# Performance work log

Measured on AMD Instinct MI355X. Metric: run time of the kernel, lower is better.

The kernel has to match this reference:

```python
import jax, jax.numpy as jnp
import numpy as np

B, CQ, CKV, H, W = 16, 512, 512, 48, 48
NH = 8
HD = CQ // NH
SCALE = HD ** -0.5


def setup_inputs() -> dict:
    key = jax.random.key(0)
    ks = jax.random.split(key, 11)
    s = 0.02
    return {
        "query_features": jax.random.normal(ks[0], (B, CQ, H, W), jnp.float32),
        "key_features": jax.random.normal(ks[1], (B, CKV, H, W), jnp.float32),
        "value_features": jax.random.normal(ks[2], (B, CKV, H, W), jnp.float32),
        "Wq": jax.random.normal(ks[3], (CQ, CQ), jnp.float32) * s,
        "bq": jnp.zeros((CQ,), jnp.float32),
        "Wk": jax.random.normal(ks[4], (CQ, CKV), jnp.float32) * s,
        "bk": jnp.zeros((CQ,), jnp.float32),
        "Wv": jax.random.normal(ks[5], (CQ, CKV), jnp.float32) * s,
        "bv": jnp.zeros((CQ,), jnp.float32),
        "Wo": jax.random.normal(ks[6], (CQ, CQ), jnp.float32) * s,
        "bo": jnp.zeros((CQ,), jnp.float32),
    }


def _proj(x, Wt, b):
    # 1x1 conv == channel GEMM: (O,C) x (B,C,H,W) -> (B,O,H,W)
    return jnp.einsum('oc,bchw->bohw', Wt, x) + b[None, :, None, None]


def reference(query_features, key_features, value_features,
              Wq, bq, Wk, bk, Wv, bv, Wo, bo):
    b, cq, h, w = query_features.shape
    hw = h * w
    Q = _proj(query_features, Wq, bq).reshape(b, NH, HD, hw)
    K = _proj(key_features, Wk, bk).reshape(b, NH, HD, hw)
    V = _proj(value_features, Wv, bv).reshape(b, NH, HD, hw)
    # NOTE: faithful to source — contraction is over the SPATIAL axis d=H*W,
    # so scores are (B, NH, HD, HD) (head_dim x head_dim attention).
    scores = jnp.einsum('bnhd,bnkd->bnhk', Q, K) * SCALE
    attn = jax.nn.softmax(scores, axis=-1)
    out = jnp.einsum('bnhk,bnkd->bnhd', attn, V)  # (B, NH, HD, HW)
    out = out.reshape(b, cq, h, w)
    return _proj(out, Wo, bo)
```

## Files before the change

### kernel.cpp

```cpp
#include <hip/hip_runtime.h>
#include <hip/hip_bf16.h>

#define B_   16
#define C_   512
#define HW_  2304
#define NH_  8
#define HD_  64
#define SCALE_ 0.125f

typedef __bf16 bf16x8 __attribute__((ext_vector_type(8)));
typedef __bf16 bf16x4 __attribute__((ext_vector_type(4)));
typedef float  f32x4  __attribute__((ext_vector_type(4)));

#define MFMA16(a, b, c) __builtin_amdgcn_mfma_f32_16x16x32_bf16((a), (b), (c), 0, 0, 0)

__device__ __forceinline__ void gload_lds16(const void* g, void* l) {
    __builtin_amdgcn_global_load_lds(
        (const __attribute__((address_space(1))) unsigned int*)g,
        (__attribute__((address_space(3))) unsigned int*)l, 16, 0, 0);
}

__global__ __launch_bounds__(256) void prep(
    const float* __restrict__ X, __bf16* __restrict__ XT,
    const float* __restrict__ W, __bf16* __restrict__ Wb)
{
    const int t = threadIdx.x;
    if (blockIdx.z == 16) {
        const int bid = blockIdx.y * 18 + blockIdx.x;
        if (bid < 128) {
            const int idx = bid * 2048 + t * 8;
            const float4 f0 = *(const float4*)&W[idx];
            const float4 f1 = *(const float4*)&W[idx + 4];
            bf16x8 o;
            o[0] = (__bf16)f0.x; o[1] = (__bf16)f0.y; o[2] = (__bf16)f0.z; o[3] = (__bf16)f0.w;
            o[4] = (__bf16)f1.x; o[5] = (__bf16)f1.y; o[6] = (__bf16)f1.z; o[7] = (__bf16)f1.w;
            *(bf16x8*)&Wb[idx] = o;
        }
        return;
    }
    const int b  = blockIdx.z;
    const int c0 = blockIdx.y * 64;
    const int h0 = blockIdx.x * 128;
    const float* Xb = X + (size_t)b * C_ * HW_;
    __bf16* XTb = XT + (size_t)b * HW_ * C_;

    __shared__ float Ts[64 * 129];

    #pragma unroll
    for (int p = 0; p < 8; ++p) {
        const int c  = p * 8 + (t >> 5);
        const int hg = (t & 31) * 4;
        const float4 v = *(const float4*)&Xb[(size_t)(c0 + c) * HW_ + h0 + hg];
        Ts[c * 129 + hg + 0] = v.x;
        Ts[c * 129 + hg + 1] = v.y;
        Ts[c * 129 + hg + 2] = v.z;
        Ts[c * 129 + hg + 3] = v.w;
    }
    __syncthreads();
    #pragma unroll
    for (int p = 0; p < 4; ++p) {
        const int hw = p * 32 + (t >> 3);
        const int g  = (t & 7) * 8;
        bf16x8 o;
        #pragma unroll
        for (int e = 0; e < 8; ++e)
            o[e] = (__bf16)Ts[(g + e) * 129 + hw];
        *(bf16x8*)&XTb[(size_t)(h0 + hw) * C_ + c0 + g] = o;
    }
}

template <typename OUT_T>
__device__ __forceinline__ void gemm_body(
    const __bf16* __restrict__ XTb, const __bf16* __restrict__ Wb,
    const float* __restrict__ bias, OUT_T* __restrict__ Yb,
    int n0, int m0)
{
    __shared__ __align__(16) __bf16 As[128 * 64];
    __shared__ __align__(16) __bf16 Bs[128 * 64];

    const int t = threadIdx.x;
    const int w = t >> 6, lane = t & 63, l16 = lane & 15, q = lane >> 4;
    const int wm = w >> 1, wn = w & 1;
    const int sr = lane >> 3;
    const int sg = ((lane & 7) ^ (lane >> 3)) * 8;

    f32x4 acc[4][4] = {};

    for (int ks = 0; ks < 8; ++ks) {
        const int k0 = ks * 64;
        __syncthreads();
        #pragma unroll
        for (int p = 0; p < 4; ++p) {
            const int rb = p * 32 + w * 8;
            gload_lds16(&Wb [(size_t)(m0 + rb + sr) * C_ + k0 + sg], &As[rb * 64]);
            gload_lds16(&XTb[(size_t)(n0 + rb + sr) * C_ + k0 + sg], &Bs[rb * 64]);
        }
        __syncthreads();
        #pragma unroll
        for (int kk = 0; kk < 2; ++kk) {
            const int sw = ((kk * 4 + q) ^ (l16 & 7)) * 8;
            bf16x8 af[4], bfr[4];
            #pragma unroll
            for (int mi = 0; mi < 4; ++mi)
                af[mi] = *(bf16x8*)&As[(wm * 64 + mi * 16 + l16) * 64 + sw];
            #pragma unroll
            for (int ni = 0; ni < 4; ++ni)
                bfr[ni] = *(bf16x8*)&Bs[(wn * 64 + ni * 16 + l16) * 64 + sw];
            #pragma unroll
            for (int mi = 0; mi < 4; ++mi)
                #pragma unroll
                for (int ni = 0; ni < 4; ++ni)
                    acc[mi][ni] = MFMA16(af[mi], bfr[ni], acc[mi][ni]);
        }
    }

    #pragma unroll
    for (int mi = 0; mi < 4; ++mi) {
        #pragma unroll
        for (int r = 0; r < 4; ++r) {
            const int m = m0 + wm * 64 + mi * 16 + q * 4 + r;
            const float bv_ = bias[m];
            #pragma unroll
            for (int ni = 0; ni < 4; ++ni) {
                const int n = n0 + wn * 64 + ni * 16 + l16;
                Yb[(size_t)m * HW_ + n] = (OUT_T)(acc[mi][ni][r] + bv_);
            }
        }
    }
}

__global__ __launch_bounds__(256) void proj_gemm(
    const __bf16* __restrict__ XT, const __bf16* __restrict__ Wb,
    const float* __restrict__ bias, __bf16* __restrict__ Y)
{
    const int b = blockIdx.z;
    gemm_body<__bf16>(XT + (size_t)b * HW_ * C_, Wb, bias,
                      Y + (size_t)b * C_ * HW_, blockIdx.x * 128, blockIdx.y * 128);
}

__global__ __launch_bounds__(256) void proj_out(
    const __bf16* __restrict__ AOT, const __bf16* __restrict__ Wb,
    const float* __restrict__ bias, float* __restrict__ out)
{
    const int b = blockIdx.z;
    gemm_body<float>(AOT + (size_t)b * HW_ * C_, Wb, bias,
                     out + (size_t)b * C_ * HW_, blockIdx.x * 128, blockIdx.y * 128);
}

__global__ __launch_bounds__(256) void attn_scores_part(
    const __bf16* __restrict__ Qw, const __bf16* __restrict__ Kw,
    float* __restrict__ Sp)
{
    const int bn  = blockIdx.x;
    const int kcs = blockIdx.y;
    const __bf16* Qb = Qw + (size_t)bn * 64 * HW_;
    const __bf16* Kb = Kw + (size_t)bn * 64 * HW_;

    __shared__ __align__(16) __bf16 Qs[64 * 64];
    __shared__ __align__(16) __bf16 Ks[64 * 64];

    const int t    = threadIdx.x;
    const int w    = t >> 6;
    const int lane = t & 63;
    const int l16  = lane & 15;
    const int q    = lane >> 4;
    const int sr   = lane >> 3;
    const int sg   = ((lane & 7) ^ (lane >> 3)) * 8;

    f32x4 acc[4] = {};

    for (int it = 0; it < 9; ++it) {
        const int k0 = kcs * 576 + it * 64;
        __syncthreads();
        #pragma unroll
        for (int p = 0; p < 2; ++p) {
            const int rb = w * 16 + p * 8;
            gload_lds16(&Qb[(size_t)(rb + sr) * HW_ + k0 + sg], &Qs[rb * 64]);
            gload_lds16(&Kb[(size_t)(rb + sr) * HW_ + k0 + sg], &Ks[rb * 64]);
        }
        __syncthreads();
        #pragma unroll
        for (int kk = 0; kk < 2; ++kk) {
            const int sw = ((kk * 4 + q) ^ (l16 & 7)) * 8;
            const bf16x8 a = *(bf16x8*)&Qs[(w * 16 + l16) * 64 + sw];
            #pragma unroll
            for (int ni = 0; ni < 4; ++ni) {
                const bf16x8 bb = *(bf16x8*)&Ks[(ni * 16 + l16) * 64 + sw];
                acc[ni] = MFMA16(a, bb, acc[ni]);
            }
        }
    }

    float* S = Sp + ((size_t)kcs * 128 + bn) * 4096;
    #pragma unroll
    for (int r = 0; r < 4; ++r)
        #pragma unroll
        for (int ni = 0; ni < 4; ++ni)
            S[(w * 16 + q * 4 + r) * 64 + ni * 16 + l16] = acc[ni][r];
}

__global__ __launch_bounds__(256) void softmax_reduce(
    const float* __restrict__ Sp, __bf16* __restrict__ Pw)
{
    const int bn = blockIdx.x;
    const int t  = threadIdx.x;
    const int r  = t >> 2;
    const int c0 = (t & 3) * 16;

    float v[16];
    #pragma unroll
    for (int j = 0; j < 16; ++j) v[j] = 0.f;
    #pragma unroll
    for (int kc = 0; kc < 4; ++kc) {
        const float* s = Sp + ((size_t)kc * 128 + bn) * 4096 + r * 64 + c0;
        #pragma unroll
        for (int j4 = 0; j4 < 4; ++j4) {
            const float4 f = *(const float4*)&s[j4 * 4];
            v[j4 * 4 + 0] += f.x; v[j4 * 4 + 1] += f.y;
            v[j4 * 4 + 2] += f.z; v[j4 * 4 + 3] += f.w;
        }
    }
    float mx = -1e30f;
    #pragma unroll
    for (int j = 0; j < 16; ++j) { v[j] *= SCALE_; mx = fmaxf(mx, v[j]); }
    mx = fmaxf(mx, __shfl_xor(mx, 1));
    mx = fmaxf(mx, __shfl_xor(mx, 2));
    float s = 0.f;
    #pragma unroll
    for (int j = 0; j < 16; ++j) { v[j] = __expf(v[j] - mx); s += v[j]; }
    s += __shfl_xor(s, 1);
    s += __shfl_xor(s, 2);
    const float inv = 1.f / s;
    bf16x8 o0, o1;
    #pragma unroll
    for (int j = 0; j < 8; ++j) {
        o0[j] = (__bf16)(v[j] * inv);
        o1[j] = (__bf16)(v[8 + j] * inv);
    }
    *(bf16x8*)&Pw[(size_t)bn * 4096 + r * 64 + c0]     = o0;
    *(bf16x8*)&Pw[(size_t)bn * 4096 + r * 64 + c0 + 8] = o1;
}

__global__ __launch_bounds__(256) void attn_pv(
    const __bf16* __restrict__ Pw, const __bf16* __restrict__ Vw,
    __bf16* __restrict__ AOT, const float* __restrict__ Wo, __bf16* __restrict__ WoB)
{
    const int t = threadIdx.x;
    if (blockIdx.x == 9) {
        const int idx = blockIdx.y * 2048 + t * 8;
        const float4 f0 = *(const float4*)&Wo[idx];
        const float4 f1 = *(const float4*)&Wo[idx + 4];
        bf16x8 o;
        o[0] = (__bf16)f0.x; o[1] = (__bf16)f0.y; o[2] = (__bf16)f0.z; o[3] = (__bf16)f0.w;
        o[4] = (__bf16)f1.x; o[5] = (__bf16)f1.y; o[6] = (__bf16)f1.z; o[7] = (__bf16)f1.w;
        *(bf16x8*)&WoB[idx] = o;
        return;
    }
    const int dsl = blockIdx.x;
    const int bn  = blockIdx.y;
    const int w    = t >> 6;
    const int lane = t & 63;
    const int l16  = lane & 15;
    const int q    = lane >> 4;

    __shared__ __align__(16) __bf16 Ps[64 * 72];
    __shared__ __align__(16) __bf16 Vt[4][16 * 264];

    {
        const int row = t >> 2;
        const int kc  = (t & 3) * 16;
        *(bf16x8*)&Ps[row * 72 + kc]     = *(const bf16x8*)&Pw[(size_t)bn * 4096 + row * 64 + kc];
        *(bf16x8*)&Ps[row * 72 + kc + 8] = *(const bf16x8*)&Pw[(size_t)bn * 4096 + row * 64 + kc + 8];
    }

    const __bf16* Vb = Vw + (size_t)bn * 64 * HW_;
    const int d0w = dsl * 256 + w * 64;
    {
        const int m4 = lane & 15;
        const int kh = (lane >> 4) * 16;
        __bf16 rr[4][16];
        #pragma unroll
        for (int j = 0; j < 16; ++j) {
            const bf16x4 v = *(const bf16x4*)&Vb[(size_t)(kh + j) * HW_ + d0w + 4 * m4];
            #pragma unroll
            for (int e = 0; e < 4; ++e) rr[e][j] = v[e];
        }
        #pragma unroll
        for (int e = 0; e < 4; ++e) {
            bf16x8 s0, s1;
            #pragma unroll
            for (int j = 0; j < 8; ++j) { s0[j] = rr[e][j]; s1[j] = rr[e][8 + j]; }
            *(bf16x8*)&Vt[w][m4 * 264 + e * 64 + kh]     = s0;
            *(bf16x8*)&Vt[w][m4 * 264 + e * 64 + kh + 8] = s1;
        }
    }
    __syncthreads();

    f32x4 acc[4][4] = {};
    #pragma unroll
    for (int kk = 0; kk < 2; ++kk) {
        bf16x8 af[4], bfr[4];
        #pragma unroll
        for (int mi = 0; mi < 4; ++mi)
            af[mi] = *(bf16x8*)&Ps[(mi * 16 + l16) * 72 + kk * 32 + q * 8];
        #pragma unroll
        for (int ni = 0; ni < 4; ++ni) {
            const int dl = ni * 16 + l16;
            bfr[ni] = *(bf16x8*)&Vt[w][(dl >> 2) * 264 + (dl & 3) * 64 + kk * 32 + q * 8];
        }
        #pragma unroll
        for (int mi = 0; mi < 4; ++mi)
            #pragma unroll
            for (int ni = 0; ni < 4; ++ni)
                acc[mi][ni] = MFMA16(af[mi], bfr[ni], acc[mi][ni]);
    }

    const int bb = bn >> 3;
    const int nh = bn & 7;
    #pragma unroll
    for (int mi = 0; mi < 4; ++mi)
        #pragma unroll
        for (int ni = 0; ni < 4; ++ni) {
            const int d = d0w + ni * 16 + l16;
            bf16x4 o;
            #pragma unroll
            for (int r = 0; r < 4; ++r) o[r] = (__bf16)acc[mi][ni][r];
            *(bf16x4*)&AOT[((size_t)bb * HW_ + d) * C_ + nh * 64 + mi * 16 + q * 4] = o;
        }
}

extern "C" void kernel_launch(void* const* d_in, const int* in_sizes, int n_in,
                              void* d_out, int out_size, void* d_ws, size_t ws_size,
                              hipStream_t stream)
{
    (void)in_sizes; (void)n_in; (void)out_size; (void)ws_size;
    const float* qf = (const float*)d_in[0];
    const float* kf = (const float*)d_in[1];
    const float* vf = (const float*)d_in[2];
    const float* Wq = (const float*)d_in[3];
    const float* bq = (const float*)d_in[4];
    const float* Wk = (const float*)d_in[5];
    const float* bk = (const float*)d_in[6];
    const float* Wv = (const float*)d_in[7];
    const float* bv = (const float*)d_in[8];
    const float* Wo = (const float*)d_in[9];
    const float* bo = (const float*)d_in[10];

    const size_t QE = (size_t)B_ * C_ * HW_;
    __bf16* region0 = (__bf16*)d_ws;
    __bf16* XT  = region0;
    float*  Sp  = (float*)region0;
    __bf16* AOT = region0;
    __bf16* Qw  = region0 + QE;
    __bf16* Kw  = Qw + QE;
    __bf16* Vw  = Kw + QE;
    __bf16* slotP = Vw + QE;
    __bf16* Wb  = slotP;
    __bf16* Pw  = slotP;
    __bf16* WoB = Qw;

    prep     <<<dim3(18, 8, 17), 256, 0, stream>>>(qf, XT, Wq, Wb);
    proj_gemm<<<dim3(18, 4, 16), 256, 0, stream>>>(XT, Wb, bq, Qw);
    prep     <<<dim3(18, 8, 17), 256, 0, stream>>>(kf, XT, Wk, Wb);
    proj_gemm<<<dim3(18, 4, 16), 256, 0, stream>>>(XT, Wb, bk, Kw);
    prep     <<<dim3(18, 8, 17), 256, 0, stream>>>(vf, XT, Wv, Wb);
    proj_gemm<<<dim3(18, 4, 16), 256, 0, stream>>>(XT, Wb, bv, Vw);

    attn_scores_part<<<dim3(128, 4), 256, 0, stream>>>(Qw, Kw, Sp);
    softmax_reduce  <<<dim3(128),    256, 0, stream>>>(Sp, Pw);
    attn_pv         <<<dim3(10, 128), 256, 0, stream>>>(Pw, Vw, AOT, Wo, WoB);
    proj_out        <<<dim3(18, 4, 16), 256, 0, stream>>>(AOT, WoB, bo, (float*)d_out);
}
```

Before: 420.9 us.

## Reassociate attention via channel Gram matrix and fold projections into one weight

Instead of projecting Q, K and V over the full spatial extent, the scores are rebuilt from the Gram matrix Xk·Xq^T (C×C per batch) and the Wq/Wk weights, with bias terms handled analytically through per-channel spatial sums. The softmax output is multiplied into Wv, and the result is multiplied by Wo, giving one fused per-batch C×C weight U. A single final GEMM applies U to the value input. This removes three large spatial projection GEMMs and the intermediate Q/K/V round trips, in exchange for several small C×C GEMMs and a reordering of bf16 rounding.

```diff
diff --git a/kernel.cpp b/kernel.cpp
--- a/kernel.cpp
+++ b/kernel.cpp
@@ -5,7 +5,6 @@
 #define C_   512
 #define HW_  2304
 #define NH_  8
-#define HD_  64
 #define SCALE_ 0.125f
 
 typedef __bf16 bf16x8 __attribute__((ext_vector_type(8)));
@@ -20,24 +19,61 @@
         (__attribute__((address_space(3))) unsigned int*)l, 16, 0, 0);
 }
 
+__device__ __forceinline__ bf16x8 pack8(const float4 a, const float4 b) {
+    bf16x8 o;
+    o[0] = (__bf16)a.x; o[1] = (__bf16)a.y; o[2] = (__bf16)a.z; o[3] = (__bf16)a.w;
+    o[4] = (__bf16)b.x; o[5] = (__bf16)b.y; o[6] = (__bf16)b.z; o[7] = (__bf16)b.w;
+    return o;
+}
+
+__global__ __launch_bounds__(256) void wprep(
+    const float* __restrict__ Wq, const float* __restrict__ Wk,
+    const float* __restrict__ Wv, const float* __restrict__ Wo,
+    __bf16* __restrict__ WqB, __bf16* __restrict__ WkB,
+    __bf16* __restrict__ WvT, __bf16* __restrict__ WoB)
+{
+    const int t = threadIdx.x;
+    if (blockIdx.y < 3) {
+        const float* src = blockIdx.y == 0 ? Wq : blockIdx.y == 1 ? Wk : Wo;
+        __bf16*      dst = blockIdx.y == 0 ? WqB : blockIdx.y == 1 ? WkB : WoB;
+        const int idx = blockIdx.x * 2048 + t * 8;
+        const float4 f0 = *(const float4*)&src[idx];
+        const float4 f1 = *(const float4*)&src[idx + 4];
+        *(bf16x8*)&dst[idx] = pack8(f0, f1);
+        return;
+    }
+    if (blockIdx.x >= 64) return;
+    const int tx = blockIdx.x & 7, ty = blockIdx.x >> 3;
+    __shared__ float Ts[64 * 65];
+    {
+        const int r = t >> 2, c0 = (t & 3) * 16;
+        #pragma unroll
+        for (int j = 0; j < 4; ++j) {
+            const float4 v = *(const float4*)&Wv[(size_t)(ty * 64 + r) * C_ + tx * 64 + c0 + j * 4];
+            Ts[r * 65 + c0 + j * 4 + 0] = v.x;
+            Ts[r * 65 + c0 + j * 4 + 1] = v.y;
+            Ts[r * 65 + c0 + j * 4 + 2] = v.z;
+            Ts[r * 65 + c0 + j * 4 + 3] = v.w;
+        }
+    }
+    __syncthreads();
+    {
+        const int c = t >> 2, r0 = (t & 3) * 16;
+        bf16x8 o0, o1;
+        #pragma unroll
+        for (int j = 0; j < 8; ++j) {
+            o0[j] = (__bf16)Ts[(r0 + j) * 65 + c];
+            o1[j] = (__bf16)Ts[(r0 + 8 + j) * 65 + c];
+        }
+        *(bf16x8*)&WvT[(size_t)(tx * 64 + c) * C_ + ty * 64 + r0]     = o0;
+        *(bf16x8*)&WvT[(size_t)(tx * 64 + c) * C_ + ty * 64 + r0 + 8] = o1;
+    }
+}
+
 __global__ __launch_bounds__(256) void prep(
-    const float* __restrict__ X, __bf16* __restrict__ XT,
-    const float* __restrict__ W, __bf16* __restrict__ Wb)
-{
-    const int t = threadIdx.x;
-    if (blockIdx.z == 16) {
-        const int bid = blockIdx.y * 18 + blockIdx.x;
-        if (bid < 128) {
-            const int idx = bid * 2048 + t * 8;
-            const float4 f0 = *(const float4*)&W[idx];
-            const float4 f1 = *(const float4*)&W[idx + 4];
-            bf16x8 o;
-            o[0] = (__bf16)f0.x; o[1] = (__bf16)f0.y; o[2] = (__bf16)f0.z; o[3] = (__bf16)f0.w;
-            o[4] = (__bf16)f1.x; o[5] = (__bf16)f1.y; o[6] = (__bf16)f1.z; o[7] = (__bf16)f1.w;
-            *(bf16x8*)&Wb[idx] = o;
-        }
-        return;
-    }
+    const float* __restrict__ X, __bf16* __restrict__ XT)
+{
+    const int t  = threadIdx.x;
     const int b  = blockIdx.z;
     const int c0 = blockIdx.y * 64;
     const int h0 = blockIdx.x * 128;
@@ -69,9 +105,398 @@
     }
 }
 
-template <typename OUT_T>
+__global__ __launch_bounds__(512) void gxx(
+    const float* __restrict__ Xk, const float* __restrict__ Xq,
+    __bf16* __restrict__ Gp, float* __restrict__ xksum, float* __restrict__ xqsum)
+{
+    const int i    = blockIdx.x;
+    const int xcd  = i & 7, slot = i >> 3;
+    const int b    = xcd + 8 * (slot & 1);
+    const int xy   = slot >> 1;
+    const int n0   = (xy & 3) * 128;
+    const int m0   = (xy >> 2) * 128;
+
+    __shared__ __align__(16) __bf16 As[128 * 64];
+    __shared__ __align__(16) __bf16 Bs[128 * 64];
+
+    const int t = threadIdx.x, w = t >> 6, lane = t & 63, l16 = lane & 15, q = lane >> 4;
+    const int wm = w >> 1, wn = w & 1;
+    const int r = t >> 2, qq = t & 3;
+
+    const float* Ap = Xk + (size_t)b * C_ * HW_ + (size_t)(m0 + r) * HW_ + qq * 16;
+    const float* Bp = Xq + (size_t)b * C_ * HW_ + (size_t)(n0 + r) * HW_ + qq * 16;
+
+    float4 av[4], bv[4];
+    #pragma unroll
+    for (int j = 0; j < 4; ++j) {
+        av[j] = *(const float4*)&Ap[j * 4];
+        bv[j] = *(const float4*)&Bp[j * 4];
+    }
+
+    const bool doA = (n0 == 0), doB = (m0 == 0);
+    float sA = 0.f, sB = 0.f;
+    f32x4 acc[2][4] = {};
+
+    for (int ks = 0; ks < 36; ++ks) {
+        if (ks) __syncthreads();
+        if (doA) {
+            #pragma unroll
+            for (int j = 0; j < 4; ++j) sA += av[j].x + av[j].y + av[j].z + av[j].w;
+        }
+        if (doB) {
+            #pragma unroll
+            for (int j = 0; j < 4; ++j) sB += bv[j].x + bv[j].y + bv[j].z + bv[j].w;
+        }
+        #pragma unroll
+        for (int jj = 0; jj < 2; ++jj) {
+            const int g  = qq * 2 + jj;
+            const int sw = (g ^ (r & 7)) * 8;
+            *(bf16x8*)&As[r * 64 + sw] = pack8(av[jj * 2], av[jj * 2 + 1]);
+            *(bf16x8*)&Bs[r * 64 + sw] = pack8(bv[jj * 2], bv[jj * 2 + 1]);
+        }
+        __syncthreads();
+        if (ks + 1 < 36) {
+            const int off = (ks + 1) * 64;
+            #pragma unroll
+            for (int j = 0; j < 4; ++j) {
+                av[j] = *(const float4*)&Ap[off + j * 4];
+                bv[j] = *(const float4*)&Bp[off + j * 4];
+            }
+        }
+        #pragma unroll
+        for (int kk = 0; kk < 2; ++kk) {
+            const int sw = ((kk * 4 + q) ^ (l16 & 7)) * 8;
+            bf16x8 af[2], bfr[4];
+            #pragma unroll
+            for (int mi = 0; mi < 2; ++mi)
+                af[mi] = *(bf16x8*)&As[(wm * 32 + mi * 16 + l16) * 64 + sw];
+            #pragma unroll
+            for (int ni = 0; ni < 4; ++ni)
+                bfr[ni] = *(bf16x8*)&Bs[(wn * 64 + ni * 16 + l16) * 64 + sw];
+            #pragma unroll
+            for (int mi = 0; mi < 2; ++mi)
+                #pragma unroll
+                for (int ni = 0; ni < 4; ++ni)
+                    acc[mi][ni] = MFMA16(af[mi], bfr[ni], acc[mi][ni]);
+        }
+    }
+
+    if (doA) {
+        float s = sA; s += __shfl_xor(s, 1); s += __shfl_xor(s, 2);
+        if (qq == 0) xksum[b * C_ + m0 + r] = s;
+    }
+    if (doB) {
+        float s = sB; s += __shfl_xor(s, 1); s += __shfl_xor(s, 2);
+        if (qq == 0) xqsum[b * C_ + n0 + r] = s;
+    }
+
+    __bf16* Gb = Gp + (size_t)b * C_ * C_;
+    #pragma unroll
+    for (int mi = 0; mi < 2; ++mi)
+        #pragma unroll
+        for (int rr = 0; rr < 4; ++rr) {
+            const int m = m0 + wm * 32 + mi * 16 + q * 4 + rr;
+            #pragma unroll
+            for (int ni = 0; ni < 4; ++ni) {
+                const int n = n0 + wn * 64 + ni * 16 + l16;
+                Gb[(size_t)m * C_ + n] = (__bf16)acc[mi][ni][rr];
+            }
+        }
+}
+
+__global__ __launch_bounds__(512) void scoresk(
+    const __bf16* __restrict__ Gp, const __bf16* __restrict__ WqB,
+    const __bf16* __restrict__ WkB, const float* __restrict__ xqsum,
+    const float* __restrict__ xksum, const float* __restrict__ bq,
+    const float* __restrict__ bk, __bf16* __restrict__ P)
+{
+    const int i  = blockIdx.x;
+    const int b  = (i & 7) + 8 * ((i >> 3) & 1);
+    const int nh = i >> 4;
+
+    __shared__ __align__(16) __bf16 Gs[512 * 64];
+    __shared__ __align__(16) __bf16 Ws[64 * 64];
+    __shared__ float Ss[64 * 64];
+    __shared__ float aqs[64], aks[64];
+
+    const int t = threadIdx.x, w = t >> 6, lane = t & 63, l16 = lane & 15, q = lane >> 4;
+
+    {
+        const int h = t >> 3, seg = (t & 7) * 64;
+        const __bf16* wr1 = WqB + (size_t)(nh * 64 + h) * C_ + seg;
+        const __bf16* wr2 = WkB + (size_t)(nh * 64 + h) * C_ + seg;
+        const float* x1 = xqsum + b * C_ + seg;
+        const float* x2 = xksum + b * C_ + seg;
+        float s1 = 0.f, s2 = 0.f;
+        #pragma unroll
+        for (int e = 0; e < 64; e += 8) {
+            const bf16x8 v1 = *(const bf16x8*)&wr1[e];
+            const bf16x8 v2 = *(const bf16x8*)&wr2[e];
+            #pragma unroll
+            for (int j = 0; j < 8; ++j) {
+                s1 += (float)v1[j] * x1[e + j];
+                s2 += (float)v2[j] * x2[e + j];
+            }
+        }
+        s1 += __shfl_xor(s1, 1); s1 += __shfl_xor(s1, 2); s1 += __shfl_xor(s1, 4);
+        s2 += __shfl_xor(s2, 1); s2 += __shfl_xor(s2, 2); s2 += __shfl_xor(s2, 4);
+        if ((t & 7) == 0) { aqs[h] = s1; aks[h] = s2; }
+    }
+
+    const int hf = w >> 1, ch = w & 1;
+    const __bf16* Gb = Gp + (size_t)b * C_ * C_;
+    f32x4 acc[16] = {};
+
+    for (int ks = 0; ks < 8; ++ks) {
+        const int k0 = ks * 64;
+        __syncthreads();
+        {
+            const int row = t >> 3;
+            const int sg  = ((lane & 7) ^ (row & 7)) * 8;
+            gload_lds16(&WqB[(size_t)(nh * 64 + row) * C_ + k0 + sg], &Ws[(w * 8) * 64]);
+        }
+        #pragma unroll
+        for (int p = 0; p < 8; ++p) {
+            const int row = p * 64 + w * 8 + (lane >> 3);
+            const int sg  = ((lane & 7) ^ (row & 7)) * 8;
+            gload_lds16(&Gb[(size_t)row * C_ + k0 + sg], &Gs[(p * 64 + w * 8) * 64]);
+        }
+        __syncthreads();
+        #pragma unroll
+        for (int kk = 0; kk < 2; ++kk) {
+            const int sw = ((kk * 4 + q) ^ (l16 & 7)) * 8;
+            const bf16x8 a = *(const bf16x8*)&Ws[(hf * 16 + l16) * 64 + sw];
+            #pragma unroll
+            for (int ni = 0; ni < 16; ++ni) {
+                const bf16x8 g = *(const bf16x8*)&Gs[(ch * 256 + ni * 16 + l16) * 64 + sw];
+                acc[ni] = MFMA16(a, g, acc[ni]);
+            }
+        }
+    }
+
+    __syncthreads();
+    #pragma unroll
+    for (int ni = 0; ni < 16; ++ni) {
+        const int c2 = ch * 256 + ni * 16 + l16;
+        #pragma unroll
+        for (int rr = 0; rr < 4; ++rr) {
+            const int h = hf * 16 + q * 4 + rr;
+            Gs[h * 512 + (((c2 >> 3) ^ (h & 7)) << 3) + (c2 & 7)] = (__bf16)acc[ni][rr];
+        }
+    }
+    __syncthreads();
+
+    f32x4 sacc[2] = {};
+    const int kf0 = (w & 1) * 2;
+    for (int ks = 0; ks < 8; ++ks) {
+        if (ks) __syncthreads();
+        {
+            const int row = t >> 3;
+            const int sg  = ((lane & 7) ^ (row & 7)) * 8;
+            gload_lds16(&WkB[(size_t)(nh * 64 + row) * C_ + ks * 64 + sg], &Ws[(w * 8) * 64]);
+        }
+        __syncthreads();
+        #pragma unroll
+        for (int kk = 0; kk < 2; ++kk) {
+            const int h = hf * 16 + l16;
+            const int g = ks * 8 + kk * 4 + q;
+            const bf16x8 a = *(const bf16x8*)&Gs[h * 512 + ((g ^ (h & 7)) << 3)];
+            const int swb = ((kk * 4 + q) ^ (l16 & 7)) * 8;
+            #pragma unroll
+            for (int kf = 0; kf < 2; ++kf) {
+                const bf16x8 bb = *(const bf16x8*)&Ws[((kf0 + kf) * 16 + l16) * 64 + swb];
+                sacc[kf] = MFMA16(a, bb, sacc[kf]);
+            }
+        }
+    }
+
+    #pragma unroll
+    for (int kf = 0; kf < 2; ++kf)
+        #pragma unroll
+        for (int rr = 0; rr < 4; ++rr)
+            Ss[(hf * 16 + q * 4 + rr) * 64 + (kf0 + kf) * 16 + l16] = sacc[kf][rr];
+    __syncthreads();
+
+    {
+        const int h = t >> 3, j0 = (t & 7) * 8;
+        const float bqv = bq[nh * 64 + h];
+        const float aqv = aqs[h];
+        float v[8];
+        float mx = -1e30f;
+        #pragma unroll
+        for (int j = 0; j < 8; ++j) {
+            const int k = j0 + j;
+            const float bkv = bk[nh * 64 + k];
+            v[j] = SCALE_ * (Ss[h * 64 + k] + aqv * bkv + bqv * (aks[k] + (float)HW_ * bkv));
+            mx = fmaxf(mx, v[j]);
+        }
+        mx = fmaxf(mx, __shfl_xor(mx, 1));
+        mx = fmaxf(mx, __shfl_xor(mx, 2));
+        mx = fmaxf(mx, __shfl_xor(mx, 4));
+        float sum = 0.f;
+        #pragma unroll
+        for (int j = 0; j < 8; ++j) { v[j] = __expf(v[j] - mx); sum += v[j]; }
+        sum += __shfl_xor(sum, 1); sum += __shfl_xor(sum, 2); sum += __shfl_xor(sum, 4);
+        const float inv = 1.f / sum;
+        bf16x8 o;
+        #pragma unroll
+        for (int j = 0; j < 8; ++j) o[j] = (__bf16)(v[j] * inv);
+        *(bf16x8*)&P[(((size_t)b * NH_ + nh) * 64 + h) * 64 + j0] = o;
+    }
+}
+
+__global__ __launch_bounds__(512) void pwv(
+    const __bf16* __restrict__ P, const __bf16* __restrict__ WvT,
+    const float* __restrict__ bv, __bf16* __restrict__ W2T, float* __restrict__ Bb)
+{
+    const int n = blockIdx.x, b = blockIdx.y;
+    __shared__ __align__(16) __bf16 Ps[64 * 64];
+    __shared__ __align__(16) __bf16 Vs[512 * 64];
+    __shared__ __align__(16) __bf16 W2s[8][64 * 72];
+
+    const int t = threadIdx.x, w = t >> 6, lane = t & 63, l16 = lane & 15, q = lane >> 4;
+
+    {
+        const int row = t >> 3;
+        const int sg  = ((lane & 7) ^ (row & 7)) * 8;
+        gload_lds16(&P[(((size_t)b * NH_ + n) * 64 + row) * 64 + sg], &Ps[(w * 8) * 64]);
+    }
+    #pragma unroll
+    for (int p = 0; p < 8; ++p) {
+        const int row = p * 64 + w * 8 + (lane >> 3);
+        const int sg  = ((lane & 7) ^ (row & 7)) * 8;
+        gload_lds16(&WvT[(size_t)row * C_ + n * 64 + sg], &Vs[(p * 64 + w * 8) * 64]);
+    }
+    __syncthreads();
+
+    {
+        const int h = t >> 3, g = t & 7;
+        const bf16x8 pv = *(const bf16x8*)&Ps[h * 64 + ((g ^ (h & 7)) << 3)];
+        float s = 0.f;
+        #pragma unroll
+        for (int j = 0; j < 8; ++j) s += (float)pv[j] * bv[n * 64 + g * 8 + j];
+        s += __shfl_xor(s, 1); s += __shfl_xor(s, 2); s += __shfl_xor(s, 4);
+        if (g == 0) Bb[b * C_ + n * 64 + h] = s;
+    }
+
+    f32x4 acc[4][4] = {};
+    #pragma unroll
+    for (int kk = 0; kk < 2; ++kk) {
+        const int sw = ((kk * 4 + q) ^ (l16 & 7)) * 8;
+        bf16x8 af[4], bfr[4];
+        #pragma unroll
+        for (int hf = 0; hf < 4; ++hf)
+            af[hf] = *(const bf16x8*)&Ps[(hf * 16 + l16) * 64 + sw];
+        #pragma unroll
+        for (int ni = 0; ni < 4; ++ni)
+            bfr[ni] = *(const bf16x8*)&Vs[(w * 64 + ni * 16 + l16) * 64 + sw];
+        #pragma unroll
+        for (int hf = 0; hf < 4; ++hf)
+            #pragma unroll
+            for (int ni = 0; ni < 4; ++ni)
+                acc[hf][ni] = MFMA16(af[hf], bfr[ni], acc[hf][ni]);
+    }
+
+    #pragma unroll
+    for (int hf = 0; hf < 4; ++hf)
+        #pragma unroll
+        for (int ni = 0; ni < 4; ++ni) {
+            const int cl = ni * 16 + l16;
+            bf16x4 o;
+            #pragma unroll
+            for (int rr = 0; rr < 4; ++rr) o[rr] = (__bf16)acc[hf][ni][rr];
+            *(bf16x4*)&W2s[w][cl * 72 + hf * 16 + q * 4] = o;
+        }
+    __syncthreads();
+    #pragma unroll
+    for (int p = 0; p < 8; ++p) {
+        const int cl = p * 8 + (lane >> 3);
+        const int g  = lane & 7;
+        const bf16x8 v = *(const bf16x8*)&W2s[w][cl * 72 + g * 8];
+        *(bf16x8*)&W2T[((size_t)b * C_ + w * 64 + cl) * C_ + n * 64 + g * 8] = v;
+    }
+}
+
+__global__ __launch_bounds__(512) void ugemm(
+    const __bf16* __restrict__ W2T, const __bf16* __restrict__ WoB,
+    __bf16* __restrict__ U, const float* __restrict__ Bb,
+    const float* __restrict__ bo, float* __restrict__ fb)
+{
+    const int b  = blockIdx.z;
+    const int n0 = blockIdx.x * 128;
+    const int m0 = blockIdx.y * 128;
+    const __bf16* Bn = W2T + (size_t)b * C_ * C_;
+
+    __shared__ __align__(16) __bf16 As[128 * 64];
+    __shared__ __align__(16) __bf16 Bs[128 * 64];
+
+    const int t = threadIdx.x, w = t >> 6, lane = t & 63, l16 = lane & 15, q = lane >> 4;
+    const int wm = w >> 1, wn = w & 1;
+    const int sr = lane >> 3;
+    const int sg = ((lane & 7) ^ sr) * 8;
+
+    f32x4 acc[2][4] = {};
+    for (int ks = 0; ks < 8; ++ks) {
+        const int k0 = ks * 64;
+        __syncthreads();
+        #pragma unroll
+        for (int p = 0; p < 2; ++p) {
+            const int rb = p * 64 + w * 8;
+            gload_lds16(&WoB[(size_t)(m0 + rb + sr) * C_ + k0 + sg], &As[rb * 64]);
+            gload_lds16(&Bn [(size_t)(n0 + rb + sr) * C_ + k0 + sg], &Bs[rb * 64]);
+        }
+        __syncthreads();
+        #pragma unroll
+        for (int kk = 0; kk < 2; ++kk) {
+            const int sw = ((kk * 4 + q) ^ (l16 & 7)) * 8;
+            bf16x8 af[2], bfr[4];
+            #pragma unroll
+            for (int mi = 0; mi < 2; ++mi)
+                af[mi] = *(bf16x8*)&As[(wm * 32 + mi * 16 + l16) * 64 + sw];
+            #pragma unroll
+            for (int ni = 0; ni < 4; ++ni)
+                bfr[ni] = *(bf16x8*)&Bs[(wn * 64 + ni * 16 + l16) * 64 + sw];
+            #pragma unroll
+            for (int mi = 0; mi < 2; ++mi)
+                #pragma unroll
+                for (int ni = 0; ni < 4; ++ni)
+                    acc[mi][ni] = MFMA16(af[mi], bfr[ni], acc[mi][ni]);
+        }
+    }
+
+    __bf16* Ub = U + (size_t)b * C_ * C_;
+    #pragma unroll
+    for (int mi = 0; mi < 2; ++mi)
+        #pragma unroll
+        for (int rr = 0; rr < 4; ++rr) {
+            const int m = m0 + wm * 32 + mi * 16 + q * 4 + rr;
+            #pragma unroll
+            for (int ni = 0; ni < 4; ++ni) {
+                const int n = n0 + wn * 64 + ni * 16 + l16;
+                Ub[(size_t)m * C_ + n] = (__bf16)acc[mi][ni][rr];
+            }
+        }
+
+    if (blockIdx.x == 0) {
+        const int o   = m0 + (t >> 2);
+        const int seg = (t & 3) * 128;
+        const __bf16* wr = WoB + (size_t)o * C_ + seg;
+        const float* be = Bb + b * C_ + seg;
+        float s = 0.f;
+        #pragma unroll
+        for (int e = 0; e < 128; e += 8) {
+            const bf16x8 v = *(const bf16x8*)&wr[e];
+            #pragma unroll
+            for (int j = 0; j < 8; ++j) s += (float)v[j] * be[e + j];
+        }
+        s += __shfl_xor(s, 1); s += __shfl_xor(s, 2);
+        if ((t & 3) == 0) fb[b * C_ + o] = s + bo[o];
+    }
+}
+
+template <typename OUT_T, int OSTR, bool BIAS>
 __device__ __forceinline__ void gemm_body(
-    const __bf16* __restrict__ XTb, const __bf16* __restrict__ Wb,
+    const __bf16* __restrict__ Bn, const __bf16* __restrict__ Am,
     const float* __restrict__ bias, OUT_T* __restrict__ Yb,
     int n0, int m0)
 {
@@ -92,8 +517,8 @@
         #pragma unroll
         for (int p = 0; p < 4; ++p) {
             const int rb = p * 32 + w * 8;
-            gload_lds16(&Wb [(size_t)(m0 + rb + sr) * C_ + k0 + sg], &As[rb * 64]);
-            gload_lds16(&XTb[(size_t)(n0 + rb + sr) * C_ + k0 + sg], &Bs[rb * 64]);
+            gload_lds16(&Am[(size_t)(m0 + rb + sr) * C_ + k0 + sg], &As[rb * 64]);
+            gload_lds16(&Bn[(size_t)(n0 + rb + sr) * C_ + k0 + sg], &Bs[rb * 64]);
         }
         __syncthreads();
         #pragma unroll
@@ -119,214 +544,24 @@
         #pragma unroll
         for (int r = 0; r < 4; ++r) {
             const int m = m0 + wm * 64 + mi * 16 + q * 4 + r;
-            const float bv_ = bias[m];
+            const float bv_ = BIAS ? bias[m] : 0.f;
             #pragma unroll
             for (int ni = 0; ni < 4; ++ni) {
                 const int n = n0 + wn * 64 + ni * 16 + l16;
-                Yb[(size_t)m * HW_ + n] = (OUT_T)(acc[mi][ni][r] + bv_);
+                Yb[(size_t)m * OSTR + n] = (OUT_T)(acc[mi][ni][r] + bv_);
             }
         }
     }
 }
 
-__global__ __launch_bounds__(256) void proj_gemm(
-    const __bf16* __restrict__ XT, const __bf16* __restrict__ Wb,
-    const float* __restrict__ bias, __bf16* __restrict__ Y)
+__global__ __launch_bounds__(256) void finalk(
+    const __bf16* __restrict__ XvT, const __bf16* __restrict__ U,
+    const float* __restrict__ fb, float* __restrict__ out)
 {
     const int b = blockIdx.z;
-    gemm_body<__bf16>(XT + (size_t)b * HW_ * C_, Wb, bias,
-                      Y + (size_t)b * C_ * HW_, blockIdx.x * 128, blockIdx.y * 128);
-}
-
-__global__ __launch_bounds__(256) void proj_out(
-    const __bf16* __restrict__ AOT, const __bf16* __restrict__ Wb,
-    const float* __restrict__ bias, float* __restrict__ out)
-{
-    const int b = blockIdx.z;
-    gemm_body<float>(AOT + (size_t)b * HW_ * C_, Wb, bias,
-                     out + (size_t)b * C_ * HW_, blockIdx.x * 128, blockIdx.y * 128);
-}
-
-__global__ __launch_bounds__(256) void attn_scores_part(
-    const __bf16* __restrict__ Qw, const __bf16* __restrict__ Kw,
-    float* __restrict__ Sp)
-{
-    const int bn  = blockIdx.x;
-    const int kcs = blockIdx.y;
-    const __bf16* Qb = Qw + (size_t)bn * 64 * HW_;
-    const __bf16* Kb = Kw + (size_t)bn * 64 * HW_;
-
-    __shared__ __align__(16) __bf16 Qs[64 * 64];
-    __shared__ __align__(16) __bf16 Ks[64 * 64];
-
-    const int t    = threadIdx.x;
-    const int w    = t >> 6;
-    const int lane = t & 63;
-    const int l16  = lane & 15;
-    const int q    = lane >> 4;
-    const int sr   = lane >> 3;
-    const int sg   = ((lane & 7) ^ (lane >> 3)) * 8;
-
-    f32x4 acc[4] = {};
-
-    for (int it = 0; it < 9; ++it) {
-        const int k0 = kcs * 576 + it * 64;
-        __syncthreads();
-        #pragma unroll
-        for (int p = 0; p < 2; ++p) {
-            const int rb = w * 16 + p * 8;
-            gload_lds16(&Qb[(size_t)(rb + sr) * HW_ + k0 + sg], &Qs[rb * 64]);
-            gload_lds16(&Kb[(size_t)(rb + sr) * HW_ + k0 + sg], &Ks[rb * 64]);
-        }
-        __syncthreads();
-        #pragma unroll
-        for (int kk = 0; kk < 2; ++kk) {
-            const int sw = ((kk * 4 + q) ^ (l16 & 7)) * 8;
-            const bf16x8 a = *(bf16x8*)&Qs[(w * 16 + l16) * 64 + sw];
-            #pragma unroll
-            for (int ni = 0; ni < 4; ++ni) {
-                const bf16x8 bb = *(bf16x8*)&Ks[(ni * 16 + l16) * 64 + sw];
-                acc[ni] = MFMA16(a, bb, acc[ni]);
-            }
-        }
-    }
-
-    float* S = Sp + ((size_t)kcs * 128 + bn) * 4096;
-    #pragma unroll
-    for (int r = 0; r < 4; ++r)
-        #pragma unroll
-        for (int ni = 0; ni < 4; ++ni)
-            S[(w * 16 + q * 4 + r) * 64 + ni * 16 + l16] = acc[ni][r];
-}
-
-__global__ __launch_bounds__(256) void softmax_reduce(
-    const float* __restrict__ Sp, __bf16* __restrict__ Pw)
-{
-    const int bn = blockIdx.x;
-    const int t  = threadIdx.x;
-    const int r  = t >> 2;
-    const int c0 = (t & 3) * 16;
-
-    float v[16];
-    #pragma unroll
-    for (int j = 0; j < 16; ++j) v[j] = 0.f;
-    #pragma unroll
-    for (int kc = 0; kc < 4; ++kc) {
-        const float* s = Sp + ((size_t)kc * 128 + bn) * 4096 + r * 64 + c0;
-        #pragma unroll
-        for (int j4 = 0; j4 < 4; ++j4) {
-            const float4 f = *(const float4*)&s[j4 * 4];
-            v[j4 * 4 + 0] += f.x; v[j4 * 4 + 1] += f.y;
-            v[j4 * 4 + 2] += f.z; v[j4 * 4 + 3] += f.w;
-        }
-    }
-    float mx = -1e30f;
-    #pragma unroll
-    for (int j = 0; j < 16; ++j) { v[j] *= SCALE_; mx = fmaxf(mx, v[j]); }
-    mx = fmaxf(mx, __shfl_xor(mx, 1));
-    mx = fmaxf(mx, __shfl_xor(mx, 2));
-    float s = 0.f;
-    #pragma unroll
-    for (int j = 0; j < 16; ++j) { v[j] = __expf(v[j] - mx); s += v[j]; }
-    s += __shfl_xor(s, 1);
-    s += __shfl_xor(s, 2);
-    const float inv = 1.f / s;
-    bf16x8 o0, o1;
-    #pragma unroll
-    for (int j = 0; j < 8; ++j) {
-        o0[j] = (__bf16)(v[j] * inv);
-        o1[j] = (__bf16)(v[8 + j] * inv);
-    }
-    *(bf16x8*)&Pw[(size_t)bn * 4096 + r * 64 + c0]     = o0;
-    *(bf16x8*)&Pw[(size_t)bn * 4096 + r * 64 + c0 + 8] = o1;
-}
-
-__global__ __launch_bounds__(256) void attn_pv(
-    const __bf16* __restrict__ Pw, const __bf16* __restrict__ Vw,
-    __bf16* __restrict__ AOT, const float* __restrict__ Wo, __bf16* __restrict__ WoB)
-{
-    const int t = threadIdx.x;
-    if (blockIdx.x == 9) {
-        const int idx = blockIdx.y * 2048 + t * 8;
-        const float4 f0 = *(const float4*)&Wo[idx];
-        const float4 f1 = *(const float4*)&Wo[idx + 4];
-        bf16x8 o;
-        o[0] = (__bf16)f0.x; o[1] = (__bf16)f0.y; o[2] = (__bf16)f0.z; o[3] = (__bf16)f0.w;
-        o[4] = (__bf16)f1.x; o[5] = (__bf16)f1.y; o[6] = (__bf16)f1.z; o[7] = (__bf16)f1.w;
-        *(bf16x8*)&WoB[idx] = o;
-        return;
-    }
-    const int dsl = blockIdx.x;
-    const int bn  = blockIdx.y;
-    const int w    = t >> 6;
-    const int lane = t & 63;
-    const int l16  = lane & 15;
-    const int q    = lane >> 4;
-
-    __shared__ __align__(16) __bf16 Ps[64 * 72];
-    __shared__ __align__(16) __bf16 Vt[4][16 * 264];
-
-    {
-        const int row = t >> 2;
-        const int kc  = (t & 3) * 16;
-        *(bf16x8*)&Ps[row * 72 + kc]     = *(const bf16x8*)&Pw[(size_t)bn * 4096 + row * 64 + kc];
-        *(bf16x8*)&Ps[row * 72 + kc + 8] = *(const bf16x8*)&Pw[(size_t)bn * 4096 + row * 64 + kc + 8];
-    }
-
-    const __bf16* Vb = Vw + (size_t)bn * 64 * HW_;
-    const int d0w = dsl * 256 + w * 64;
-    {
-        const int m4 = lane & 15;
-        const int kh = (lane >> 4) * 16;
-        __bf16 rr[4][16];
-        #pragma unroll
-        for (int j = 0; j < 16; ++j) {
-            const bf16x4 v = *(const bf16x4*)&Vb[(size_t)(kh + j) * HW_ + d0w + 4 * m4];
-            #pragma unroll
-            for (int e = 0; e < 4; ++e) rr[e][j] = v[e];
-        }
-        #pragma unroll
-        for (int e = 0; e < 4; ++e) {
-            bf16x8 s0, s1;
-            #pragma unroll
-            for (int j = 0; j < 8; ++j) { s0[j] = rr[e][j]; s1[j] = rr[e][8 + j]; }
-            *(bf16x8*)&Vt[w][m4 * 264 + e * 64 + kh]     = s0;
-            *(bf16x8*)&Vt[w][m4 * 264 + e * 64 + kh + 8] = s1;
-        }
-    }
-    __syncthreads();
-
-    f32x4 acc[4][4] = {};
-    #pragma unroll
-    for (int kk = 0; kk < 2; ++kk) {
-        bf16x8 af[4], bfr[4];
-        #pragma unroll
-        for (int mi = 0; mi < 4; ++mi)
-            af[mi] = *(bf16x8*)&Ps[(mi * 16 + l16) * 72 + kk * 32 + q * 8];
-        #pragma unroll
-        for (int ni = 0; ni < 4; ++ni) {
-            const int dl = ni * 16 + l16;
-            bfr[ni] = *(bf16x8*)&Vt[w][(dl >> 2) * 264 + (dl & 3) * 64 + kk * 32 + q * 8];
-        }
-        #pragma unroll
-        for (int mi = 0; mi < 4; ++mi)
-            #pragma unroll
-            for (int ni = 0; ni < 4; ++ni)
-                acc[mi][ni] = MFMA16(af[mi], bfr[ni], acc[mi][ni]);
-    }
-
-    const int bb = bn >> 3;
-    const int nh = bn & 7;
-    #pragma unroll
-    for (int mi = 0; mi < 4; ++mi)
-        #pragma unroll
-        for (int ni = 0; ni < 4; ++ni) {
-            const int d = d0w + ni * 16 + l16;
-            bf16x4 o;
-            #pragma unroll
-            for (int r = 0; r < 4; ++r) o[r] = (__bf16)acc[mi][ni][r];
-            *(bf16x4*)&AOT[((size_t)bb * HW_ + d) * C_ + nh * 64 + mi * 16 + q * 4] = o;
-        }
+    gemm_body<float, HW_, true>(XvT + (size_t)b * HW_ * C_, U + (size_t)b * C_ * C_,
+                                fb + b * C_, out + (size_t)b * C_ * HW_,
+                                blockIdx.x * 128, blockIdx.y * 128);
 }
 
 extern "C" void kernel_launch(void* const* d_in, const int* in_sizes, int n_in,
@@ -346,28 +581,25 @@
     const float* Wo = (const float*)d_in[9];
     const float* bo = (const float*)d_in[10];
 
-    const size_t QE = (size_t)B_ * C_ * HW_;
-    __bf16* region0 = (__bf16*)d_ws;
-    __bf16* XT  = region0;
-    float*  Sp  = (float*)region0;
-    __bf16* AOT = region0;
-    __bf16* Qw  = region0 + QE;
-    __bf16* Kw  = Qw + QE;
-    __bf16* Vw  = Kw + QE;
-    __bf16* slotP = Vw + QE;
-    __bf16* Wb  = slotP;
-    __bf16* Pw  = slotP;
-    __bf16* WoB = Qw;
-
-    prep     <<<dim3(18, 8, 17), 256, 0, stream>>>(qf, XT, Wq, Wb);
-    proj_gemm<<<dim3(18, 4, 16), 256, 0, stream>>>(XT, Wb, bq, Qw);
-    prep     <<<dim3(18, 8, 17), 256, 0, stream>>>(kf, XT, Wk, Wb);
-    proj_gemm<<<dim3(18, 4, 16), 256, 0, stream>>>(XT, Wb, bk, Kw);
-    prep     <<<dim3(18, 8, 17), 256, 0, stream>>>(vf, XT, Wv, Wb);
-    proj_gemm<<<dim3(18, 4, 16), 256, 0, stream>>>(XT, Wb, bv, Vw);
-
-    attn_scores_part<<<dim3(128, 4), 256, 0, stream>>>(Qw, Kw, Sp);
-    softmax_reduce  <<<dim3(128),    256, 0, stream>>>(Sp, Pw);
-    attn_pv         <<<dim3(10, 128), 256, 0, stream>>>(Pw, Vw, AOT, Wo, WoB);
-    proj_out        <<<dim3(18, 4, 16), 256, 0, stream>>>(AOT, WoB, bo, (float*)d_out);
-}
+    __bf16* XvT  = (__bf16*)d_ws;
+    __bf16* Gp   = XvT  + (size_t)B_ * HW_ * C_;
+    __bf16* W2T  = Gp   + (size_t)B_ * C_ * C_;
+    __bf16* U    = W2T  + (size_t)B_ * C_ * C_;
+    __bf16* WqB  = U    + (size_t)B_ * C_ * C_;
+    __bf16* WkB  = WqB  + C_ * C_;
+    __bf16* WvTb = WkB  + C_ * C_;
+    __bf16* WoB  = WvTb + C_ * C_;
+    __bf16* Pb   = WoB  + C_ * C_;
+    float*  xqs  = (float*)(Pb + (size_t)B_ * NH_ * 64 * 64);
+    float*  xks  = xqs + B_ * C_;
+    float*  Bb   = xks + B_ * C_;
+    float*  fb   = Bb  + B_ * C_;
+
+    wprep  <<<dim3(128, 4),   256, 0, stream>>>(Wq, Wk, Wv, Wo, WqB, WkB, WvTb, WoB);
+    prep   <<<dim3(18, 8, 16),256, 0, stream>>>(vf, XvT);
+    gxx    <<<dim3(256),      512, 0, stream>>>(kf, qf, Gp, xks, xqs);
+    scoresk<<<dim3(128),      512, 0, stream>>>(Gp, WqB, WkB, xqs, xks, bq, bk, Pb);
+    pwv    <<<dim3(8, 16),    512, 0, stream>>>(Pb, WvTb, bv, W2T, Bb);
+    ugemm  <<<dim3(4, 4, 16), 512, 0, stream>>>(W2T, WoB, U, Bb, bo, fb);
+    finalk <<<dim3(18, 4, 16),256, 0, stream>>>(XvT, U, fb, (float*)d_out);
+}
```

After: 395.6 us. -6.0%, faster.
